# Kernel tuning notes

Measured on AMD Instinct MI355X. Metric: run time of the kernel, lower is better.

## Reference

```python
import jax, jax.numpy as jnp
import numpy as np

COST_CLASS, COST_BBOX, COST_GIOU = 2.0, 5.0, 2.0
ALPHA, GAMMA, EPS = 0.25, 2.0, 1e-8


def box_cxcywh_to_xyxy(x):
    cx, cy, w, h = x[..., 0], x[..., 1], x[..., 2], x[..., 3]
    return jnp.stack([cx - 0.5 * w, cy - 0.5 * h, cx + 0.5 * w, cy + 0.5 * h], axis=-1)


def generalized_box_iou(b1, b2):
    # b1: [N,4], b2: [M,4] in xyxy -> [N,M]
    a1 = (b1[:, 2] - b1[:, 0]) * (b1[:, 3] - b1[:, 1])
    a2 = (b2[:, 2] - b2[:, 0]) * (b2[:, 3] - b2[:, 1])
    lt = jnp.maximum(b1[:, None, :2], b2[None, :, :2])
    rb = jnp.minimum(b1[:, None, 2:], b2[None, :, 2:])
    wh = jnp.maximum(rb - lt, 0.0)
    inter = wh[..., 0] * wh[..., 1]
    union = a1[:, None] + a2[None, :] - inter
    iou = inter / jnp.maximum(union, 1e-6)
    elt = jnp.minimum(b1[:, None, :2], b2[None, :, :2])
    erb = jnp.maximum(b1[:, None, 2:], b2[None, :, 2:])
    ewh = jnp.maximum(erb - elt, 0.0)
    encl = ewh[..., 0] * ewh[..., 1]
    return iou - (encl - union) / jnp.maximum(encl, 1e-6)


def setup_inputs() -> dict:
    key = jax.random.key(0)
    k1, k2, k3, k4 = jax.random.split(key, 4)
    bs, nq, nc, nt = 16, 900, 80, 3200
    return {
        'pred_logits': jax.random.normal(k1, (bs, nq, nc), dtype=jnp.float32),
        'pred_boxes': jax.random.uniform(k2, (bs, nq, 4), dtype=jnp.float32),
        'tgt_labels': jax.random.randint(k3, (nt,), 0, nc, dtype=jnp.int32),
        'tgt_boxes': jax.random.uniform(k4, (nt, 4), dtype=jnp.float32),
    }


def reference(pred_logits, pred_boxes, tgt_labels, tgt_boxes):
    bs, nq, nc = pred_logits.shape
    out_prob = jax.nn.sigmoid(pred_logits.reshape(bs * nq, nc))  # [N, C]
    out_bbox = pred_boxes.reshape(bs * nq, 4)                    # [N, 4]

    p = out_prob[:, tgt_labels]  # [N, M] gather by target class
    neg_cost = (1.0 - ALPHA) * p ** GAMMA * (-jnp.log(1.0 - p + EPS))
    pos_cost = ALPHA * (1.0 - p) ** GAMMA * (-jnp.log(p + EPS))
    cost_class = pos_cost - neg_cost

    # L1 cdist: [N, M]
    cost_bbox = jnp.sum(jnp.abs(out_bbox[:, None, :] - tgt_boxes[None, :, :]), axis=-1)

    cost_giou = -generalized_box_iou(box_cxcywh_to_xyxy(out_bbox), box_cxcywh_to_xyxy(tgt_boxes))

    C = COST_BBOX * cost_bbox + COST_CLASS * cost_class + COST_GIOU * cost_giou
    C = jnp.nan_to_num(C, nan=1.0)
    return C.reshape(bs, nq, -1)
```

## Files before the change

kernel.cpp:

```cpp
#include <hip/hip_runtime.h>
#include <cmath>

#define NCC   80
#define QT    8
#define BLK   256
#define VT    4
#define NT_C  3200
#define NQB_C 14400
#define CPR   (NT_C / VT)
#define NRG   (NQB_C / QT)
#define CSTR  20

typedef float f32x4 __attribute__((ext_vector_type(4)));

__device__ __forceinline__ float cls_cost(float x) {
    const float p   = 1.0f / (1.0f + __expf(-x));
    const float om  = 1.0f - p;
    const float pos = 0.25f * om * om * (-__logf(p  + 1e-8f));
    const float neg = 0.75f * p  * p  * (-__logf(om + 1e-8f));
    return 2.0f * (pos - neg) + 2.0f;
}

__global__ __launch_bounds__(BLK) void cost_fast(
    const float* __restrict__ logits,
    const float* __restrict__ pboxes,
    const int*   __restrict__ labels,
    const float* __restrict__ tboxes,
    float*       __restrict__ out)
{
    __shared__ float4 s_clsv[NCC * (CSTR / 4)];
    __shared__ float4 s_qb[2 * QT];
    float* s_cls = (float*)s_clsv;

    const int  w0   = blockIdx.x * BLK;
    const int  rg0  = w0 / CPR;
    const int  row0 = rg0 * QT;
    const bool two  = (((w0 + BLK - 1) / CPR) != rg0);

    const int w  = w0 + threadIdx.x;
    const int rg = w / CPR;
    const int c  = w - rg * CPR;
    const int j  = c * VT;
    const int g8 = (rg - rg0) * QT;

    const int4 lab4 = ((const int4*)labels)[c];
    const int labk[VT] = { lab4.x, lab4.y, lab4.z, lab4.w };
    float4 tb[VT];
    float ta[VT];
#pragma unroll
    for (int k = 0; k < VT; ++k) {
        tb[k] = ((const float4*)tboxes)[j + k];
        ta[k] = tb[k].z * tb[k].w;
    }

    {
        const int nst = (two ? 2 * QT : QT) * NCC;
        const float* src = logits + row0 * NCC;
        for (int t = threadIdx.x; t < nst; t += BLK) {
            const int ro  = t / NCC;
            const int lab = t - ro * NCC;
            s_cls[lab * CSTR + ro] = cls_cost(src[t]);
        }
    }
    const int ng = two ? 2 * QT : QT;
    if (threadIdx.x < ng) {
        s_qb[threadIdx.x] = ((const float4*)pboxes)[row0 + threadIdx.x];
    }
    __syncthreads();

    const unsigned obase = (unsigned)(rg * QT) * NT_C + (unsigned)j;

#pragma unroll 1
    for (int h = 0; h < 2; ++h) {
        const int qbase = g8 + h * 4;
        float4 c2v[VT];
#pragma unroll
        for (int k = 0; k < VT; ++k)
            c2v[k] = *(const float4*)&s_cls[labk[k] * CSTR + qbase];

        const unsigned offh = obase + (unsigned)h * 4u * NT_C;
#pragma unroll
        for (int q4 = 0; q4 < 4; ++q4) {
            const int    qi = qbase + q4;
            const float4 qb = s_qb[qi];
            const float  qa = qb.z * qb.w;
            float res[VT];
#pragma unroll
            for (int k = 0; k < VT; ++k) {
                const float c2 = c2v[k][q4];
                const float d1 = qb.x - tb[k].x;
                const float d2 = qb.y - tb[k].y;
                const float d3 = qb.z - tb[k].z;
                const float d4 = qb.w - tb[k].w;
                const float sx = qb.z + tb[k].z;
                const float sy = qb.w + tb[k].w;
                const float dxr = fmaf(0.5f, sx, -fabsf(d1));
                const float dyr = fmaf(0.5f, sy, -fabsf(d2));
                const float dx  = fminf(fminf(dxr, qb.z), tb[k].z);
                const float dy  = fminf(fminf(dyr, qb.w), tb[k].w);
                const float iw  = fmaxf(dx, 0.0f);
                const float ih  = fmaxf(dy, 0.0f);
                const float inter = iw * ih;
                const float uni   = (qa + ta[k]) - inter;
                const float ew = sx - dx;
                const float eh = sy - dy;
                const float encl = ew * eh;
                const float r1 = __builtin_amdgcn_rcpf(fmaxf(uni,  1e-6f));
                const float r2 = __builtin_amdgcn_rcpf(fmaxf(encl, 1e-6f));
                const float l1 = (fabsf(d1) + fabsf(d2)) + (fabsf(d3) + fabsf(d4));
                float cc = fmaf(5.0f, l1, c2);
                cc = fmaf(-2.0f * inter, r1, cc);
                cc = fmaf(-2.0f * uni,  r2, cc);
                res[k] = cc;
            }
            f32x4 v = { res[0], res[1], res[2], res[3] };
            __builtin_nontemporal_store(
                v, (f32x4*)(out + offh + (unsigned)q4 * NT_C));
        }
    }
}

__global__ __launch_bounds__(BLK) void cost_generic(
    const float* __restrict__ logits, const float* __restrict__ pboxes,
    const int* __restrict__ labels, const float* __restrict__ tboxes,
    float* __restrict__ out, int NQB, int NT, int NC)
{
    extern __shared__ float smem[];
    float*  s_cls = smem;
    float4* s_qb  = (float4*)(smem + QT * NC);

    const int i0 = blockIdx.y * QT;
    const int j  = blockIdx.x * BLK + threadIdx.x;

    for (int t = threadIdx.x; t < QT * NC; t += BLK) {
        const int qi = i0 + t / NC;
        float v = 0.0f;
        if (qi < NQB) {
            const float x  = logits[qi * NC + (t % NC)];
            const float p  = 1.0f / (1.0f + __expf(-x));
            const float om = 1.0f - p;
            v = 0.25f * om * om * (-__logf(p + 1e-8f))
              - 0.75f * p * p * (-__logf(om + 1e-8f));
        }
        s_cls[t] = v;
    }
    if (threadIdx.x < QT) {
        const int qi = i0 + threadIdx.x;
        s_qb[threadIdx.x] = (qi < NQB) ? ((const float4*)pboxes)[qi]
                                       : make_float4(0.f, 0.f, 0.f, 0.f);
    }
    __syncthreads();
    if (j >= NT) return;

    const float4 tb = ((const float4*)tboxes)[j];
    const int   lab = labels[j];
    const float tx0 = tb.x - 0.5f * tb.z, tx1 = tb.x + 0.5f * tb.z;
    const float ty0 = tb.y - 0.5f * tb.w, ty1 = tb.y + 0.5f * tb.w;
    const float ta  = tb.z * tb.w;

#pragma unroll
    for (int q = 0; q < QT; ++q) {
        const float4 qb = s_qb[q];
        const float ccls = s_cls[q * NC + lab];
        const float l1 = fabsf(qb.x - tb.x) + fabsf(qb.y - tb.y)
                       + fabsf(qb.z - tb.z) + fabsf(qb.w - tb.w);
        const float qx0 = qb.x - 0.5f * qb.z, qx1 = qb.x + 0.5f * qb.z;
        const float qy0 = qb.y - 0.5f * qb.w, qy1 = qb.y + 0.5f * qb.w;
        const float qa  = qb.z * qb.w;
        const float ltx = fmaxf(qx0, tx0), lty = fmaxf(qy0, ty0);
        const float rbx = fminf(qx1, tx1), rby = fminf(qy1, ty1);
        const float iw = fmaxf(rbx - ltx, 0.f), ih = fmaxf(rby - lty, 0.f);
        const float inter = iw * ih;
        const float uni   = qa + ta - inter;
        const float iou   = inter * __builtin_amdgcn_rcpf(fmaxf(uni, 1e-6f));
        const float ex0 = fminf(qx0, tx0), ey0 = fminf(qy0, ty0);
        const float ex1 = fmaxf(qx1, tx1), ey1 = fmaxf(qy1, ty1);
        const float ew = fmaxf(ex1 - ex0, 0.f), eh = fmaxf(ey1 - ey0, 0.f);
        const float encl = ew * eh;
        const float giou = iou - (encl - uni) * __builtin_amdgcn_rcpf(fmaxf(encl, 1e-6f));
        float cc = 5.0f * l1 + 2.0f * ccls - 2.0f * giou;
        cc = (cc == cc) ? cc : 1.0f;
        const int qi = i0 + q;
        if (qi < NQB) out[(size_t)qi * NT + j] = cc;
    }
}

extern "C" void kernel_launch(void* const* d_in, const int* in_sizes, int n_in,
                              void* d_out, int out_size, void* d_ws, size_t ws_size,
                              hipStream_t stream) {
    const float* logits = (const float*)d_in[0];
    const float* pboxes = (const float*)d_in[1];
    const int*   labels = (const int*)d_in[2];
    const float* tboxes = (const float*)d_in[3];
    float*       out    = (float*)d_out;

    const int nqb = in_sizes[1] / 4;
    const int nt  = in_sizes[2];
    const int nc  = in_sizes[0] / nqb;

    if (nqb == NQB_C && nt == NT_C && nc == NCC) {
        const int nblk = (NRG * CPR) / BLK;
        hipLaunchKernelGGL(cost_fast, dim3(nblk), dim3(BLK), 0, stream,
                           logits, pboxes, labels, tboxes, out);
    } else {
        dim3 grid((nt + BLK - 1) / BLK, (nqb + QT - 1) / QT);
        size_t sm = QT * nc * sizeof(float) + QT * sizeof(float4);
        hipLaunchKernelGGL(cost_generic, grid, dim3(BLK), sm, stream,
                           logits, pboxes, labels, tboxes, out, nqb, nt, nc);
    }
}
```

Before: 52.43 us.

## Assign one query row-group per block and loop over all target columns

Each block now owns one 8-query row group and loops across all 800 target column chunks, instead of each block covering 256 column chunks that may straddle two row groups. The class-cost shared-memory table is built once per row group rather than once or twice per 256-thread slice, which removes redundant sigmoid/log work and shared-memory fill. The cost is a smaller grid of 1800 blocks, each doing a longer serial loop with an uneven last iteration (800/256 is not whole). Target boxes and labels are reloaded from global memory on every loop iteration.

```diff
diff --git a/kernel.cpp b/kernel.cpp
--- a/kernel.cpp
+++ b/kernel.cpp
@@ -29,93 +29,88 @@
     float*       __restrict__ out)
 {
     __shared__ float4 s_clsv[NCC * (CSTR / 4)];
-    __shared__ float4 s_qb[2 * QT];
+    __shared__ float4 s_qb[QT];
     float* s_cls = (float*)s_clsv;
 
-    const int  w0   = blockIdx.x * BLK;
-    const int  rg0  = w0 / CPR;
-    const int  row0 = rg0 * QT;
-    const bool two  = (((w0 + BLK - 1) / CPR) != rg0);
-
-    const int w  = w0 + threadIdx.x;
-    const int rg = w / CPR;
-    const int c  = w - rg * CPR;
-    const int j  = c * VT;
-    const int g8 = (rg - rg0) * QT;
-
-    const int4 lab4 = ((const int4*)labels)[c];
-    const int labk[VT] = { lab4.x, lab4.y, lab4.z, lab4.w };
-    float4 tb[VT];
-    float ta[VT];
-#pragma unroll
-    for (int k = 0; k < VT; ++k) {
-        tb[k] = ((const float4*)tboxes)[j + k];
-        ta[k] = tb[k].z * tb[k].w;
-    }
+    const int rg   = blockIdx.x;
+    const int row0 = rg * QT;
 
     {
-        const int nst = (two ? 2 * QT : QT) * NCC;
         const float* src = logits + row0 * NCC;
-        for (int t = threadIdx.x; t < nst; t += BLK) {
+        for (int t = threadIdx.x; t < QT * NCC; t += BLK) {
             const int ro  = t / NCC;
             const int lab = t - ro * NCC;
             s_cls[lab * CSTR + ro] = cls_cost(src[t]);
         }
     }
-    const int ng = two ? 2 * QT : QT;
-    if (threadIdx.x < ng) {
+    if (threadIdx.x < QT) {
         s_qb[threadIdx.x] = ((const float4*)pboxes)[row0 + threadIdx.x];
     }
     __syncthreads();
 
-    const unsigned obase = (unsigned)(rg * QT) * NT_C + (unsigned)j;
+    const unsigned rowbase = (unsigned)row0 * NT_C;
+
+    for (int cc = threadIdx.x; cc < CPR; cc += BLK) {
+        const int j = cc * VT;
+
+        const int4 lab4 = ((const int4*)labels)[cc];
+        const int labk[VT] = { lab4.x, lab4.y, lab4.z, lab4.w };
+        float4 tb[VT];
+        float ta[VT];
+#pragma unroll
+        for (int k = 0; k < VT; ++k) {
+            tb[k] = ((const float4*)tboxes)[j + k];
+            ta[k] = tb[k].z * tb[k].w;
+        }
+
+        const unsigned obase = rowbase + (unsigned)j;
 
 #pragma unroll 1
-    for (int h = 0; h < 2; ++h) {
-        const int qbase = g8 + h * 4;
-        float4 c2v[VT];
-#pragma unroll
-        for (int k = 0; k < VT; ++k)
-            c2v[k] = *(const float4*)&s_cls[labk[k] * CSTR + qbase];
-
-        const unsigned offh = obase + (unsigned)h * 4u * NT_C;
-#pragma unroll
-        for (int q4 = 0; q4 < 4; ++q4) {
-            const int    qi = qbase + q4;
-            const float4 qb = s_qb[qi];
-            const float  qa = qb.z * qb.w;
-            float res[VT];
-#pragma unroll
-            for (int k = 0; k < VT; ++k) {
-                const float c2 = c2v[k][q4];
-                const float d1 = qb.x - tb[k].x;
-                const float d2 = qb.y - tb[k].y;
-                const float d3 = qb.z - tb[k].z;
-                const float d4 = qb.w - tb[k].w;
-                const float sx = qb.z + tb[k].z;
-                const float sy = qb.w + tb[k].w;
-                const float dxr = fmaf(0.5f, sx, -fabsf(d1));
-                const float dyr = fmaf(0.5f, sy, -fabsf(d2));
-                const float dx  = fminf(fminf(dxr, qb.z), tb[k].z);
-                const float dy  = fminf(fminf(dyr, qb.w), tb[k].w);
-                const float iw  = fmaxf(dx, 0.0f);
-                const float ih  = fmaxf(dy, 0.0f);
-                const float inter = iw * ih;
-                const float uni   = (qa + ta[k]) - inter;
-                const float ew = sx - dx;
-                const float eh = sy - dy;
-                const float encl = ew * eh;
-                const float r1 = __builtin_amdgcn_rcpf(fmaxf(uni,  1e-6f));
-                const float r2 = __builtin_amdgcn_rcpf(fmaxf(encl, 1e-6f));
-                const float l1 = (fabsf(d1) + fabsf(d2)) + (fabsf(d3) + fabsf(d4));
-                float cc = fmaf(5.0f, l1, c2);
-                cc = fmaf(-2.0f * inter, r1, cc);
-                cc = fmaf(-2.0f * uni,  r2, cc);
-                res[k] = cc;
+        for (int h = 0; h < 2; ++h) {
+            const int qbase = h * 4;
+            float4 c2v[VT];
+#pragma unroll
+            for (int k = 0; k < VT; ++k)
+                c2v[k] = *(const float4*)&s_cls[labk[k] * CSTR + qbase];
+
+            const unsigned offh = obase + (unsigned)h * 4u * NT_C;
+#pragma unroll
+            for (int q4 = 0; q4 < 4; ++q4) {
+                const float4 qb = s_qb[qbase + q4];
+                const float  qa = qb.z * qb.w;
+                float res[VT];
+#pragma unroll
+                for (int k = 0; k < VT; ++k) {
+                    const float c2 = c2v[k][q4];
+                    const float d1 = qb.x - tb[k].x;
+                    const float d2 = qb.y - tb[k].y;
+                    const float d3 = qb.z - tb[k].z;
+                    const float d4 = qb.w - tb[k].w;
+                    const float sx = qb.z + tb[k].z;
+                    const float sy = qb.w + tb[k].w;
+                    const float dxr = fmaf(0.5f, sx, -fabsf(d1));
+                    const float dyr = fmaf(0.5f, sy, -fabsf(d2));
+                    const float dx  = fminf(fminf(dxr, qb.z), tb[k].z);
+                    const float dy  = fminf(fminf(dyr, qb.w), tb[k].w);
+                    const float iw  = fmaxf(dx, 0.0f);
+                    const float ih  = fmaxf(dy, 0.0f);
+                    const float inter = iw * ih;
+                    const float uni   = (qa + ta[k]) - inter;
+                    const float ew = sx - dx;
+                    const float eh = sy - dy;
+                    const float encl = ew * eh;
+                    const float r1 = __builtin_amdgcn_rcpf(fmaxf(uni,  1e-6f));
+                    const float r2 = __builtin_amdgcn_rcpf(fmaxf(encl, 1e-6f));
+                    const float l1 = (fabsf(d1) + fabsf(d2)) + (fabsf(d3) + fabsf(d4));
+                    float cc2 = fmaf(5.0f, l1, c2);
+                    cc2 = fmaf(-2.0f * inter, r1, cc2);
+                    cc2 = fmaf(-2.0f * uni,  r2, cc2);
+                    res[k] = cc2;
+                }
+                f32x4 v = { res[0], res[1], res[2], res[3] };
+                __builtin_nontemporal_store(
+                    v, (f32x4*)(out + offh + (unsigned)q4 * NT_C));
             }
-            f32x4 v = { res[0], res[1], res[2], res[3] };
-            __builtin_nontemporal_store(
-                v, (f32x4*)(out + offh + (unsigned)q4 * NT_C));
         }
     }
 }
@@ -199,8 +194,7 @@
     const int nc  = in_sizes[0] / nqb;
 
     if (nqb == NQB_C && nt == NT_C && nc == NCC) {
-        const int nblk = (NRG * CPR) / BLK;
-        hipLaunchKernelGGL(cost_fast, dim3(nblk), dim3(BLK), 0, stream,
+        hipLaunchKernelGGL(cost_fast, dim3(NRG), dim3(BLK), 0, stream,
                            logits, pboxes, labels, tboxes, out);
     } else {
         dim3 grid((nt + BLK - 1) / BLK, (nqb + QT - 1) / QT);
```

Result: slower. 53.58 us (+2.2%).
